# Performance work log

Measured on AMD Instinct MI355X. Metric: run time of the kernel, lower is better.

Reference implementation:

```python
import jax, jax.numpy as jnp
import numpy as np

B, S, D, H = 4, 2048, 1024, 16
HD = D // H
BITS = 8
LEVELS = 2 ** BITS - 1          # number of negative log2 levels
SCALING = 32.0 / 16.0           # lora alpha / rank for 8-bit adapter
NEG_INF = -1e9


def log_fake_quant(x, reduce_axes):
    """Per-channel log-domain fake quantization with straight-through estimator.
    Scale = per-channel max-abs; magnitudes snapped to power-of-two fractions of scale."""
    s = jnp.maximum(jnp.max(jnp.abs(x), axis=reduce_axes, keepdims=True), 1e-8)
    ratio = jnp.clip(jnp.abs(x) / s, 2.0 ** (-LEVELS), 1.0)
    e = jnp.round(jnp.log2(ratio))                      # in [-LEVELS, 0]
    q = jnp.sign(x) * s * jnp.exp2(e)
    return x + jax.lax.stop_gradient(q - x)             # STE


def cpt_linear(x, W, b, lA, lB):
    """CPTLinear: fake-quantized activation/weight GEMM + bias + LoRA on the fp input."""
    xq = log_fake_quant(x, tuple(range(x.ndim - 1)))     # per last-dim channel
    Wq = log_fake_quant(W, (1,))                         # per output row (channel_dim=0)
    out = xq @ Wq.T + b
    return out + (x @ lA @ lB) * SCALING


def setup_inputs() -> dict:
    key = jax.random.key(0)
    ks = jax.random.split(key, 8)
    causal = jnp.tril(jnp.ones((S, S), dtype=bool))
    mask = jnp.where(causal, 0.0, NEG_INF).astype(jnp.float32)[None, None]  # [1,1,S,S]
    return {
        "hidden_states": jax.random.normal(ks[0], (B, S, D), jnp.float32),
        "attention_mask": mask,
        "W_attn": jax.random.normal(ks[1], (3 * D, D), jnp.float32) * 0.02,
        "b_attn": jnp.zeros((3 * D,), jnp.float32),
        "lA_attn": jax.random.normal(ks[2], (D, 16), jnp.float32) * 0.01,
        "lB_attn": jax.random.normal(ks[3], (16, 3 * D), jnp.float32) * 0.01,
        "W_proj": jax.random.normal(ks[4], (D, D), jnp.float32) * 0.02,
        "b_proj": jnp.zeros((D,), jnp.float32),
        "lA_proj": jax.random.normal(ks[5], (D, 16), jnp.float32) * 0.01,
        "lB_proj": jax.random.normal(ks[6], (16, D), jnp.float32) * 0.01,
    }


def reference(hidden_states, attention_mask, W_attn, b_attn, lA_attn, lB_attn,
              W_proj, b_proj, lA_proj, lB_proj):
    qkv = cpt_linear(hidden_states, W_attn, b_attn, lA_attn, lB_attn)  # [B,S,3D]
    q, k, v = jnp.split(qkv, 3, axis=-1)

    def to_heads(t):
        return t.reshape(B, S, H, HD).transpose(0, 2, 1, 3)            # [B,H,S,HD]

    q, k, v = to_heads(q), to_heads(k), to_heads(v)
    scores = jnp.einsum("bhqd,bhkd->bhqk", q, k) / np.float32(np.sqrt(HD))
    scores = scores + attention_mask
    attn = jax.nn.softmax(scores, axis=-1)                             # dropout: eval mode (identity)
    out = jnp.einsum("bhqk,bhkd->bhqd", attn, v)
    out = out.transpose(0, 2, 1, 3).reshape(B, S, D)
    return cpt_linear(out, W_proj, b_proj, lA_proj, lB_proj)
```

## Files before the change

### kernel.cpp

```cpp
#include <hip/hip_runtime.h>

#define SS 2048
#define DD 1024
#define DQKV 3072
#define KP 1088
#define NT64 17
#define MTOT 8192
#define QKSZ ((size_t)MTOT * DD)
#define SCL 0.18033688011112042f

typedef unsigned short us;
typedef __attribute__((ext_vector_type(8))) short bf16x8;
typedef __attribute__((ext_vector_type(4))) float f32x4;
typedef __attribute__((ext_vector_type(4))) unsigned u32x4;

#define WAITVM(N) asm volatile("s_waitcnt vmcnt(" #N ")" ::: "memory")
#define WAITLGKM0 asm volatile("s_waitcnt lgkmcnt(0)" ::: "memory")

__device__ __forceinline__ us f2bf(float f) {
    unsigned u = __float_as_uint(f);
    return (us)((u + 0x7fffu + ((u >> 16) & 1u)) >> 16);
}
__device__ __forceinline__ float bf2f(us h) { return __uint_as_float(((unsigned)h) << 16); }
__device__ __forceinline__ void split2(float q, us& h, us& l) {
    h = f2bf(q); l = f2bf(q - bf2f(h));
}
__device__ __forceinline__ unsigned cvtpk(float lo, float hi) {
    unsigned r;
    asm("v_cvt_pk_bf16_f32 %0, %1, %2" : "=v"(r) : "v"(lo), "v"(hi));
    return r;
}

__device__ __forceinline__ int logq_e(float ax, float s) {
    int e = 0;
    if (ax < s) {
        double r = (double)ax / (double)s;
        int ex;
        double mant = frexp(r, &ex);
        e = (mant >= 0.70710678118654752440) ? ex : ex - 1;
        e = (e < -255) ? -255 : e;
    }
    return e;
}
__device__ __forceinline__ float logq_exact(float x, float s) {
    float ax = fabsf(x);
    if (ax == 0.f) return copysignf(0.f, x);
    return copysignf(ldexpf(s, logq_e(ax, s)), x);
}

__device__ __forceinline__ void gll16(const void* g, void* l) {
    __builtin_amdgcn_global_load_lds(
        (const __attribute__((address_space(1))) void*)g,
        (__attribute__((address_space(3))) void*)l, 16, 0, 0);
}


__global__ void k_zero(unsigned* p, int n) {
    int i = blockIdx.x * 256 + threadIdx.x;
    if (i < n) p[i] = 0u;
}

__global__ void k_colmax(const float* __restrict__ x, unsigned* __restrict__ smax) {
    int c = blockIdx.x * 256 + threadIdx.x;
    int r0 = blockIdx.y * 128;
    float m = 0.f;
    for (int r = 0; r < 128; ++r) m = fmaxf(m, fabsf(x[(size_t)(r0 + r) * DD + c]));
    atomicMax(smax + c, __float_as_uint(m));
}

__global__ __launch_bounds__(256) void k_quant_lora(const float* __restrict__ x,
                                                    const unsigned* __restrict__ smax,
                                                    const float* __restrict__ lA,
                                                    us* __restrict__ xq) {
    __shared__ float red[4][16];
    int m = blockIdx.x, tx = threadIdx.x;
    int lane = tx & 63, w = tx >> 6;
    float4 xv = ((const float4*)(x + (size_t)m * DD))[tx];
    int c = tx * 4;
    float vv[4] = {xv.x, xv.y, xv.z, xv.w};
    ushort4 qh;
    us* ph = (us*)&qh;
#pragma unroll
    for (int j = 0; j < 4; ++j) {
        float s = fmaxf(__uint_as_float(smax[c + j]), 1e-8f);
        float sh = bf2f(f2bf(s));
        float ax = fabsf(vv[j]);
        if (ax == 0.f) ph[j] = (us)((__float_as_uint(vv[j]) >> 16) & 0x8000u);
        else ph[j] = f2bf(copysignf(ldexpf(sh, logq_e(ax, s)), vv[j]));
    }
    *(ushort4*)(xq + (size_t)m * KP + c) = qh;
    float acc[16];
#pragma unroll
    for (int r = 0; r < 16; ++r) acc[r] = 0.f;
#pragma unroll
    for (int j = 0; j < 4; ++j) {
        float xs = vv[j];
        const float4* lr = (const float4*)(lA + (size_t)(c + j) * 16);
        float4 a0 = lr[0], a1 = lr[1], a2 = lr[2], a3 = lr[3];
        acc[0] += xs * a0.x; acc[1] += xs * a0.y; acc[2] += xs * a0.z; acc[3] += xs * a0.w;
        acc[4] += xs * a1.x; acc[5] += xs * a1.y; acc[6] += xs * a1.z; acc[7] += xs * a1.w;
        acc[8] += xs * a2.x; acc[9] += xs * a2.y; acc[10] += xs * a2.z; acc[11] += xs * a2.w;
        acc[12] += xs * a3.x; acc[13] += xs * a3.y; acc[14] += xs * a3.z; acc[15] += xs * a3.w;
    }
#pragma unroll
    for (int msk = 1; msk < 64; msk <<= 1)
#pragma unroll
        for (int r = 0; r < 16; ++r) acc[r] += __shfl_xor(acc[r], msk);
    if (lane == 0)
#pragma unroll
        for (int r = 0; r < 16; ++r) red[w][r] = acc[r];
    __syncthreads();
    if (tx < 16) {
        float v = 2.0f * (red[0][tx] + red[1][tx] + red[2][tx] + red[3][tx]);
        us h, l; split2(v, h, l);
        xq[(size_t)m * KP + 1024 + tx] = h;
        xq[(size_t)m * KP + 1040 + tx] = l;
    } else if (tx == 16) {
        xq[(size_t)m * KP + 1056] = 0x3F80;
    } else if (tx < 48) {
        xq[(size_t)m * KP + 1040 + tx] = 0;
    }
}

__global__ __launch_bounds__(256) void k_quant_w(const float* __restrict__ W, const float* __restrict__ lB,
                                                 const float* __restrict__ bias,
                                                 const unsigned* __restrict__ smax,
                                                 us* __restrict__ wh, us* __restrict__ wl, int Nn) {
    __shared__ float red[4];
    int n = blockIdx.x, tx = threadIdx.x;
    int lane = tx & 63, w = tx >> 6;
    float4 wv = ((const float4*)(W + (size_t)n * DD))[tx];
    float m4 = fmaxf(fmaxf(fabsf(wv.x), fabsf(wv.y)), fmaxf(fabsf(wv.z), fabsf(wv.w)));
#pragma unroll
    for (int msk = 1; msk < 64; msk <<= 1) m4 = fmaxf(m4, __shfl_xor(m4, msk));
    if (lane == 0) red[w] = m4;
    __syncthreads();
    float t = fmaxf(fmaxf(fmaxf(red[0], red[1]), fmaxf(red[2], red[3])), 1e-8f);
    float vv[4] = {wv.x, wv.y, wv.z, wv.w};
    int c = tx * 4;
    ushort4 qh, ql;
    us* ph = (us*)&qh; us* pl = (us*)&ql;
#pragma unroll
    for (int j = 0; j < 4; ++j) {
        float s = fmaxf(__uint_as_float(smax[c + j]), 1e-8f);
        float sh = bf2f(f2bf(s));
        float rho = (s - sh) / sh;
        float q = logq_exact(vv[j], t);
        float wp = q + q * rho;
        split2(wp, ph[j], pl[j]);
    }
    *(ushort4*)(wh + (size_t)n * KP + c) = qh;
    *(ushort4*)(wl + (size_t)n * KP + c) = ql;
    if (tx < 64) {
        us h = 0, l = 0;
        if (tx < 32) { int r = tx & 15; split2(lB[(size_t)r * Nn + n], h, l); }
        else if (tx == 32) split2(bias[n], h, l);
        wh[(size_t)n * KP + 1024 + tx] = h;
        wl[(size_t)n * KP + 1024 + tx] = l;
    }
}


template <int MODE>
__global__ __launch_bounds__(512, 2) void k_gemm(const us* __restrict__ Aq_,
                                                 const us* __restrict__ Bh_, const us* __restrict__ Bl_,
                                                 float* __restrict__ C, int Nn,
                                                 us* __restrict__ Khg, us* __restrict__ Klg,
                                                 float* __restrict__ vbuf) {
    __shared__ us LA[2][16384];
    __shared__ us LBh[2][8192];
    __shared__ us LBl[2][8192];
    int tid = threadIdx.x;
    int bm = blockIdx.x, bn = blockIdx.y;
    int lane = tid & 63, w = tid >> 6;
    int wm = w >> 2, wn = w & 3;
    int l15 = lane & 15, l4 = lane >> 4;
    int srow = tid >> 3;
    int gsrc = ((tid & 7) ^ (srow & 7)) * 8;
    const us* aP  = Aq_ + (size_t)(bm * 256 + srow) * KP + gsrc;
    const us* bhP = Bh_ + (size_t)(bn * 128 + srow) * KP + gsrc;
    const us* blP = Bl_ + (size_t)(bn * 128 + srow) * KP + gsrc;
    f32x4 zero4 = {0.f, 0.f, 0.f, 0.f};
    f32x4 acc[8][2];
#pragma unroll
    for (int i = 0; i < 8; ++i) { acc[i][0] = zero4; acc[i][1] = zero4; }

#define GSTAGE(buf, kt)                                               \
    do {                                                              \
        int k0_ = (kt) * 64;                                          \
        gll16(aP + k0_,                    &LA[(buf)][0]     + tid * 8); \
        gll16(aP + (size_t)64  * KP + k0_, &LA[(buf)][4096]  + tid * 8); \
        gll16(aP + (size_t)128 * KP + k0_, &LA[(buf)][8192]  + tid * 8); \
        gll16(aP + (size_t)192 * KP + k0_, &LA[(buf)][12288] + tid * 8); \
        gll16(bhP + k0_,                   &LBh[(buf)][0]    + tid * 8); \
        gll16(bhP + (size_t)64 * KP + k0_, &LBh[(buf)][4096] + tid * 8); \
        gll16(blP + k0_,                   &LBl[(buf)][0]    + tid * 8); \
        gll16(blP + (size_t)64 * KP + k0_, &LBl[(buf)][4096] + tid * 8); \
    } while (0)

    GSTAGE(0, 0);
    GSTAGE(1, 1);
    WAITVM(8);
    __builtin_amdgcn_s_barrier();
    __builtin_amdgcn_sched_barrier(0);

    int gsw0 = ((l4)     ^ (l15 & 7)) * 8;
    int gsw1 = ((4 + l4) ^ (l15 & 7)) * 8;
    int cur = 0;
    for (int kt = 0; kt < NT64; ++kt) {
        const us* A0  = &LA[cur][0];
        const us* Bh0 = &LBh[cur][0];
        const us* Bl0 = &LBl[cur][0];
        bf16x8 a0[8], b0h[2], b0l[2];
#pragma unroll
        for (int i = 0; i < 8; ++i)
            a0[i] = *(const bf16x8*)(A0 + (wm * 128 + i * 16 + l15) * 64 + gsw0);
#pragma unroll
        for (int i = 0; i < 2; ++i) {
            b0h[i] = *(const bf16x8*)(Bh0 + (wn * 32 + i * 16 + l15) * 64 + gsw0);
            b0l[i] = *(const bf16x8*)(Bl0 + (wn * 32 + i * 16 + l15) * 64 + gsw0);
        }
        __builtin_amdgcn_s_setprio(1);
#pragma unroll
        for (int mi = 0; mi < 8; ++mi)
#pragma unroll
            for (int ni = 0; ni < 2; ++ni) {
                acc[mi][ni] = __builtin_amdgcn_mfma_f32_16x16x32_bf16(a0[mi], b0h[ni], acc[mi][ni], 0, 0, 0);
                acc[mi][ni] = __builtin_amdgcn_mfma_f32_16x16x32_bf16(a0[mi], b0l[ni], acc[mi][ni], 0, 0, 0);
            }
        __builtin_amdgcn_s_setprio(0);
        bf16x8 a1[8], b1h[2], b1l[2];
#pragma unroll
        for (int i = 0; i < 8; ++i)
            a1[i] = *(const bf16x8*)(A0 + (wm * 128 + i * 16 + l15) * 64 + gsw1);
#pragma unroll
        for (int i = 0; i < 2; ++i) {
            b1h[i] = *(const bf16x8*)(Bh0 + (wn * 32 + i * 16 + l15) * 64 + gsw1);
            b1l[i] = *(const bf16x8*)(Bl0 + (wn * 32 + i * 16 + l15) * 64 + gsw1);
        }
        WAITLGKM0;
        __builtin_amdgcn_sched_barrier(0);
        __builtin_amdgcn_s_barrier();
        __builtin_amdgcn_sched_barrier(0);
        if (kt + 2 < NT64) GSTAGE(cur, kt + 2);
        __builtin_amdgcn_s_setprio(1);
#pragma unroll
        for (int mi = 0; mi < 8; ++mi)
#pragma unroll
            for (int ni = 0; ni < 2; ++ni) {
                acc[mi][ni] = __builtin_amdgcn_mfma_f32_16x16x32_bf16(a1[mi], b1h[ni], acc[mi][ni], 0, 0, 0);
                acc[mi][ni] = __builtin_amdgcn_mfma_f32_16x16x32_bf16(a1[mi], b1l[ni], acc[mi][ni], 0, 0, 0);
            }
        __builtin_amdgcn_s_setprio(0);
        if (kt + 2 < NT64) { WAITVM(8); } else { WAITVM(0); }
        __builtin_amdgcn_s_barrier();
        __builtin_amdgcn_sched_barrier(0);
        cur ^= 1;
    }
#undef GSTAGE

    int plane = bn >> 3;
#pragma unroll
    for (int mi = 0; mi < 8; ++mi) {
#pragma unroll
        for (int ni = 0; ni < 2; ++ni) {
            int ncol = bn * 128 + wn * 32 + ni * 16 + l15;
            size_t mbase = (size_t)bm * 256 + wm * 128 + mi * 16 + l4 * 4;
#pragma unroll
            for (int rr = 0; rr < 4; ++rr) {
                float v = acc[mi][ni][rr];
                size_t m = mbase + rr;
                if (MODE == 0) {
                    C[m * (size_t)Nn + ncol] = v;
                } else {
                    int cc = ncol & 1023;
                    if (plane == 0) {
                        C[m * DD + cc] = v;
                    } else if (plane == 2) {
                        vbuf[m * DD + cc] = v;
                    } else {
                        us hh, ll; split2(v * SCL, hh, ll);
                        size_t d = ((size_t)((m >> 11) * 16 + (cc >> 6)) * SS + (m & 2047)) * 64 + (cc & 63);
                        Khg[d] = hh; Klg[d] = ll;
                    }
                }
            }
        }
    }
}


__global__ __launch_bounds__(256) void k_transpose_v(const float* __restrict__ vbuf,
                                                     us* __restrict__ vth, us* __restrict__ vtl) {
    __shared__ us th[64][72], tl[64][72];
    int st = blockIdx.x, bh = blockIdx.y;
    int bb = bh >> 4, h = bh & 15;
    int s0 = st * 64, tid = threadIdx.x;
    int sl = tid >> 2, c0 = (tid & 3) * 16;
    const float* src = vbuf + (size_t)(bb * SS + s0 + sl) * DD + h * 64 + c0;
#pragma unroll
    for (int j4 = 0; j4 < 4; ++j4) {
        float4 v = *(const float4*)(src + j4 * 4);
        float vv[4] = {v.x, v.y, v.z, v.w};
#pragma unroll
        for (int j = 0; j < 4; ++j) {
            us hh, ll; split2(vv[j], hh, ll);
            th[c0 + j4 * 4 + j][sl] = hh;
            tl[c0 + j4 * 4 + j][sl] = ll;
        }
    }
    __syncthreads();
#pragma unroll
    for (int p = 0; p < 2; ++p) {
        int gidx = p * 256 + tid;
        int hd = gidx >> 3, g = gidx & 7;
        int base = (g >> 2) * 32 + (g & 3) * 4;
        ushort4 a, b2, c, d2;
        a.x = th[hd][base];      a.y = th[hd][base + 1];  a.z = th[hd][base + 2];  a.w = th[hd][base + 3];
        b2.x = th[hd][base + 16]; b2.y = th[hd][base + 17]; b2.z = th[hd][base + 18]; b2.w = th[hd][base + 19];
        c.x = tl[hd][base];      c.y = tl[hd][base + 1];  c.z = tl[hd][base + 2];  c.w = tl[hd][base + 3];
        d2.x = tl[hd][base + 16]; d2.y = tl[hd][base + 17]; d2.z = tl[hd][base + 18]; d2.w = tl[hd][base + 19];
        size_t dof = ((size_t)bh * 64 + hd) * SS + s0 + g * 8;
        *(ushort4*)(vth + dof) = a;  *(ushort4*)(vth + dof + 4) = b2;
        *(ushort4*)(vtl + dof) = c;  *(ushort4*)(vtl + dof + 4) = d2;
    }
}


__global__ __launch_bounds__(512, 2) void k_attn(float* qo,
                                                 const us* __restrict__ Khg, const us* __restrict__ Klg,
                                                 const us* __restrict__ vth, const us* __restrict__ vtl) {
    __shared__ us L[2][16384];
    int bh = blockIdx.x;
    int qt = (int)(gridDim.y - 1) - blockIdx.y;
    int b = bh >> 4, h = bh & 15;
    int q0 = qt * 128;
    int tid = threadIdx.x, w = tid >> 6, lane = tid & 63;
    int l15 = lane & 15, l4 = lane >> 4;
    int qw = q0 + w * 16;
    int swz = l15 & 7;

    bf16x8 qh[2], ql[2];
#pragma unroll
    for (int hf = 0; hf < 2; ++hf) {
        const float* qp = qo + (size_t)(b * SS + qw + l15) * DD + h * 64 + hf * 32 + l4 * 8;
        float4 a = *(const float4*)qp;
        float4 c = *(const float4*)(qp + 4);
        float vv[8] = {a.x, a.y, a.z, a.w, c.x, c.y, c.z, c.w};
        bf16x8 hq, lq;
#pragma unroll
        for (int j = 0; j < 8; ++j) {
            us hh = f2bf(vv[j]);
            hq[j] = (short)hh;
            lq[j] = (short)f2bf(vv[j] - bf2f(hh));
        }
        qh[hf] = hq; ql[hf] = lq;
    }

    f32x4 zero4 = {0.f, 0.f, 0.f, 0.f};
    f32x4 of[4];
#pragma unroll
    for (int j = 0; j < 4; ++j) of[j] = zero4;
    float mrow = -1e30f, lrowp = 0.f;

    int r0 = tid >> 3, sl0 = (tid & 7) ^ (r0 & 7);
    int koff0 = (bh * SS + r0) * 64 + sl0 * 8;
    int voff0 = (bh * 64 + r0) * SS + sl0 * 8;

    int ntiles = qt * 2 + 2;

#define STAGE(buf, tt)                                           \
    do {                                                         \
        int kv_ = (tt) * 64;                                     \
        us* D_ = &L[(buf)][0];                                   \
        int kadd_ = kv_ << 6;                                    \
        gll16(Khg + koff0 + kadd_, D_ + tid * 8);                \
        gll16(Klg + koff0 + kadd_, D_ + 4096 + tid * 8);         \
        gll16(vth + voff0 + kv_, D_ + 8192 + tid * 8);           \
        gll16(vtl + voff0 + kv_, D_ + 12288 + tid * 8);          \
    } while (0)

    STAGE(0, 0);
    STAGE(1, 1);
    int cur = 0;

    for (int t = 0; t < ntiles; ++t) {
        int kv0 = t * 64;
        if (t + 1 < ntiles) WAITVM(4); else WAITVM(0);
        __builtin_amdgcn_s_barrier();

        if (kv0 <= qw + 15) {
            const us* Lc = &L[cur][0];

            f32x4 sf[4];
#pragma unroll
            for (int i = 0; i < 4; ++i) sf[i] = zero4;
            __builtin_amdgcn_s_setprio(1);
#pragma unroll
            for (int kb = 0; kb < 4; ++kb) {
                int rbase = (kb * 16 + l15) * 64;
#pragma unroll
                for (int hf = 0; hf < 2; ++hf) {
                    int off = rbase + (((hf * 4 + l4) ^ swz) * 8);
                    bf16x8 kh = *(const bf16x8*)(Lc + off);
                    bf16x8 kl = *(const bf16x8*)(Lc + 4096 + off);
                    sf[kb] = __builtin_amdgcn_mfma_f32_16x16x32_bf16(kh, qh[hf], sf[kb], 0, 0, 0);
                    sf[kb] = __builtin_amdgcn_mfma_f32_16x16x32_bf16(kh, ql[hf], sf[kb], 0, 0, 0);
                    sf[kb] = __builtin_amdgcn_mfma_f32_16x16x32_bf16(kl, qh[hf], sf[kb], 0, 0, 0);
                }
            }
            __builtin_amdgcn_s_setprio(0);

            bool diag = (kv0 + 63 > qw);
            u32x4 PH[2], PL[2];
            {
                float pv[16];
                if (diag) {
                    int qg = qw + l15;
#pragma unroll
                    for (int kb = 0; kb < 4; ++kb)
#pragma unroll
                        for (int rr = 0; rr < 4; ++rr) {
                            int kvg = kv0 + kb * 16 + l4 * 4 + rr;
                            pv[kb * 4 + rr] = (kvg > qg) ? -1e30f : sf[kb][rr];
                        }
                } else {
#pragma unroll
                    for (int kb = 0; kb < 4; ++kb)
#pragma unroll
                        for (int rr = 0; rr < 4; ++rr)
                            pv[kb * 4 + rr] = sf[kb][rr];
                }
                float t0 = fmaxf(fmaxf(pv[0], pv[1]), pv[2]);
                float t1 = fmaxf(fmaxf(pv[3], pv[4]), pv[5]);
                float t2 = fmaxf(fmaxf(pv[6], pv[7]), pv[8]);
                float t3 = fmaxf(fmaxf(pv[9], pv[10]), pv[11]);
                float t4 = fmaxf(fmaxf(pv[12], pv[13]), pv[14]);
                float tmax = fmaxf(fmaxf(fmaxf(t0, t1), fmaxf(t2, t3)), fmaxf(t4, pv[15]));
                tmax = fmaxf(tmax, __shfl_xor(tmax, 16));
                tmax = fmaxf(tmax, __shfl_xor(tmax, 32));
                float mcur = mrow;
                if (!__all(tmax <= mcur + 8.0f)) {
                    float mnew = fmaxf(mcur, tmax);
                    float fac = __builtin_amdgcn_exp2f(mcur - mnew);
                    mrow = mnew; mcur = mnew;
                    lrowp *= fac;
                    float fr0 = __shfl(fac, l4 * 4 + 0);
                    float fr1 = __shfl(fac, l4 * 4 + 1);
                    float fr2 = __shfl(fac, l4 * 4 + 2);
                    float fr3 = __shfl(fac, l4 * 4 + 3);
#pragma unroll
                    for (int hb = 0; hb < 4; ++hb) {
                        of[hb][0] *= fr0; of[hb][1] *= fr1;
                        of[hb][2] *= fr2; of[hb][3] *= fr3;
                    }
                }
                float ps = 0.f;
#pragma unroll
                for (int i = 0; i < 16; ++i) {
                    pv[i] = __builtin_amdgcn_exp2f(pv[i] - mcur);
                    ps += pv[i];
                }
                lrowp += ps;
#pragma unroll
                for (int ks = 0; ks < 2; ++ks)
#pragma unroll
                    for (int c2 = 0; c2 < 4; ++c2) {
                        float p0 = pv[ks * 8 + c2 * 2], p1 = pv[ks * 8 + c2 * 2 + 1];
                        unsigned u = cvtpk(p0, p1);
                        float h0 = __uint_as_float(u << 16);
                        float h1 = __uint_as_float(u & 0xffff0000u);
                        unsigned ul = cvtpk(p0 - h0, p1 - h1);
                        PH[ks][c2] = u; PL[ks][c2] = ul;
                    }
            }

            __builtin_amdgcn_s_setprio(1);
#pragma unroll
            for (int hb = 0; hb < 4; ++hb) {
                int rbase = (hb * 16 + l15) * 64;
#pragma unroll
                for (int ks = 0; ks < 2; ++ks) {
                    int off = rbase + (((ks * 4 + l4) ^ swz) * 8);
                    bf16x8 vh = *(const bf16x8*)(Lc + 8192 + off);
                    bf16x8 vl = *(const bf16x8*)(Lc + 12288 + off);
                    bf16x8 pa = (bf16x8)PH[ks];
                    bf16x8 pb = (bf16x8)PL[ks];
                    of[hb] = __builtin_amdgcn_mfma_f32_16x16x32_bf16(pa, vh, of[hb], 0, 0, 0);
                    of[hb] = __builtin_amdgcn_mfma_f32_16x16x32_bf16(pa, vl, of[hb], 0, 0, 0);
                    of[hb] = __builtin_amdgcn_mfma_f32_16x16x32_bf16(pb, vh, of[hb], 0, 0, 0);
                }
            }
            __builtin_amdgcn_s_setprio(0);
        }

        __builtin_amdgcn_s_barrier();
        if (t + 2 < ntiles) STAGE(cur, t + 2);
        cur ^= 1;
    }
#undef STAGE

    {
        float lr = lrowp;
        lr += __shfl_xor(lr, 16);
        lr += __shfl_xor(lr, 32);
        float linv = 1.f / lr;
        float f0 = __shfl(linv, l4 * 4 + 0);
        float f1 = __shfl(linv, l4 * 4 + 1);
        float f2 = __shfl(linv, l4 * 4 + 2);
        float f3 = __shfl(linv, l4 * 4 + 3);
        int qgb = qw + l4 * 4;
#pragma unroll
        for (int hb = 0; hb < 4; ++hb) {
            int col = h * 64 + hb * 16 + l15;
            qo[((size_t)(b * SS + qgb + 0)) * DD + col] = of[hb][0] * f0;
            qo[((size_t)(b * SS + qgb + 1)) * DD + col] = of[hb][1] * f1;
            qo[((size_t)(b * SS + qgb + 2)) * DD + col] = of[hb][2] * f2;
            qo[((size_t)(b * SS + qgb + 3)) * DD + col] = of[hb][3] * f3;
        }
    }
}


extern "C" void kernel_launch(void* const* d_in, const int* in_sizes, int n_in,
                              void* d_out, int out_size, void* d_ws, size_t ws_size,
                              hipStream_t stream) {
    const float* hidden  = (const float*)d_in[0];
    const float* W_attn  = (const float*)d_in[2];
    const float* b_attn  = (const float*)d_in[3];
    const float* lA_attn = (const float*)d_in[4];
    const float* lB_attn = (const float*)d_in[5];
    const float* W_proj  = (const float*)d_in[6];
    const float* b_proj  = (const float*)d_in[7];
    const float* lA_proj = (const float*)d_in[8];
    const float* lB_proj = (const float*)d_in[9];
    float* out = (float*)d_out;

    char* ws = (char*)d_ws;
    unsigned* s1 = (unsigned*)(ws);
    unsigned* s2 = (unsigned*)(ws + 4096);
    us* xq  = (us*)(ws + 8192);
    us* vth = xq;
    us* wh1 = (us*)(ws + 8192 + 17825792);
    us* wl1 = (us*)(ws + 8192 + 17825792 + 6684672);
    us* wh2 = (us*)(ws + 8192 + 17825792 + 2 * 6684672);
    us* wl2 = (us*)(ws + 8192 + 17825792 + 2 * 6684672 + 2228224);
    char* pbase = ws + 8192 + 17825792 + 2 * 6684672 + 2 * 2228224;
    float* qbuf = (float*)pbase;
    float* vbuf = (float*)(pbase + 33554432);
    us* Khg = (us*)(pbase + 2 * (size_t)33554432);
    us* Klg = (us*)(pbase + 2 * (size_t)33554432 + 16777216);
    us* vtl = (us*)(pbase + 2 * (size_t)33554432 + 2 * (size_t)16777216);

    k_zero<<<8, 256, 0, stream>>>(s1, 2048);

    k_colmax<<<dim3(4, 64), 256, 0, stream>>>(hidden, s1);
    k_quant_lora<<<MTOT, 256, 0, stream>>>(hidden, s1, lA_attn, xq);
    k_quant_w<<<3072, 256, 0, stream>>>(W_attn, lB_attn, b_attn, s1, wh1, wl1, 3072);
    k_gemm<1><<<dim3(32, 24), 512, 0, stream>>>(xq, wh1, wl1, qbuf, DQKV, Khg, Klg, vbuf);

    k_transpose_v<<<dim3(32, 64), 256, 0, stream>>>(vbuf, vth, vtl);
    k_attn<<<dim3(64, 16), 512, 0, stream>>>(qbuf, Khg, Klg, vth, vtl);

    k_colmax<<<dim3(4, 64), 256, 0, stream>>>(qbuf, s2);
    k_quant_lora<<<MTOT, 256, 0, stream>>>(qbuf, s2, lA_proj, xq);
    k_quant_w<<<1024, 256, 0, stream>>>(W_proj, lB_proj, b_proj, s2, wh2, wl2, 1024);
    k_gemm<0><<<dim3(32, 8), 512, 0, stream>>>(xq, wh2, wl2, out, DD, nullptr, nullptr, nullptr);
}
```

Measured before the change: 447.4 us.

## Halve GEMM K-tile to 32 to raise occupancy and use float log-quant

Shrinks the GEMM K-step from 64 to 32, halving LDS buffers so launch bounds can request 4 blocks per CU instead of 2, with a matching XOR swizzle for 32-wide rows. The loop now does one MFMA phase per iteration, with two barriers. The log-quant exponent is computed with a float frexp plus a double-precision squared-boundary correction, replacing the double division. The aim is more resident waves to hide latency, at the cost of twice as many barriers and loop iterations and a tighter register budget that could cause spills with 16 accumulators.

```diff
diff --git a/kernel.cpp b/kernel.cpp
--- a/kernel.cpp
+++ b/kernel.cpp
@@ -4,7 +4,7 @@
 #define DD 1024
 #define DQKV 3072
 #define KP 1088
-#define NT64 17
+#define NT32 34
 #define MTOT 8192
 #define QKSZ ((size_t)MTOT * DD)
 #define SCL 0.18033688011112042f
@@ -34,11 +34,15 @@
 __device__ __forceinline__ int logq_e(float ax, float s) {
     int e = 0;
     if (ax < s) {
-        double r = (double)ax / (double)s;
         int ex;
-        double mant = frexp(r, &ex);
-        e = (mant >= 0.70710678118654752440) ? ex : ex - 1;
-        e = (e < -255) ? -255 : e;
+        float m = frexpf(ax / s, &ex);
+        int k = (m >= 0.70710678f) ? ex : ex - 1;
+        double ax2 = (double)ax * (double)ax;
+        double s2 = (double)s * (double)s;
+        if (ax2 >= ldexp(s2, 2 * k + 1)) k += 1;
+        else if (ax2 < ldexp(s2, 2 * k - 1)) k -= 1;
+        if (k > 0) k = 0;
+        e = (k < -255) ? -255 : k;
     }
     return e;
 }
@@ -162,21 +166,21 @@
 
 
 template <int MODE>
-__global__ __launch_bounds__(512, 2) void k_gemm(const us* __restrict__ Aq_,
+__global__ __launch_bounds__(512, 4) void k_gemm(const us* __restrict__ Aq_,
                                                  const us* __restrict__ Bh_, const us* __restrict__ Bl_,
                                                  float* __restrict__ C, int Nn,
                                                  us* __restrict__ Khg, us* __restrict__ Klg,
                                                  float* __restrict__ vbuf) {
-    __shared__ us LA[2][16384];
-    __shared__ us LBh[2][8192];
-    __shared__ us LBl[2][8192];
+    __shared__ us LA[2][8192];
+    __shared__ us LBh[2][4096];
+    __shared__ us LBl[2][4096];
     int tid = threadIdx.x;
     int bm = blockIdx.x, bn = blockIdx.y;
     int lane = tid & 63, w = tid >> 6;
     int wm = w >> 2, wn = w & 3;
     int l15 = lane & 15, l4 = lane >> 4;
-    int srow = tid >> 3;
-    int gsrc = ((tid & 7) ^ (srow & 7)) * 8;
+    int srow = tid >> 2;
+    int gsrc = ((tid & 3) ^ ((srow ^ (srow >> 2)) & 3)) * 8;
     const us* aP  = Aq_ + (size_t)(bm * 256 + srow) * KP + gsrc;
     const us* bhP = Bh_ + (size_t)(bn * 128 + srow) * KP + gsrc;
     const us* blP = Bl_ + (size_t)(bn * 128 + srow) * KP + gsrc;
@@ -185,41 +189,40 @@
 #pragma unroll
     for (int i = 0; i < 8; ++i) { acc[i][0] = zero4; acc[i][1] = zero4; }
 
-#define GSTAGE(buf, kt)                                               \
-    do {                                                              \
-        int k0_ = (kt) * 64;                                          \
-        gll16(aP + k0_,                    &LA[(buf)][0]     + tid * 8); \
-        gll16(aP + (size_t)64  * KP + k0_, &LA[(buf)][4096]  + tid * 8); \
-        gll16(aP + (size_t)128 * KP + k0_, &LA[(buf)][8192]  + tid * 8); \
-        gll16(aP + (size_t)192 * KP + k0_, &LA[(buf)][12288] + tid * 8); \
-        gll16(bhP + k0_,                   &LBh[(buf)][0]    + tid * 8); \
-        gll16(bhP + (size_t)64 * KP + k0_, &LBh[(buf)][4096] + tid * 8); \
-        gll16(blP + k0_,                   &LBl[(buf)][0]    + tid * 8); \
-        gll16(blP + (size_t)64 * KP + k0_, &LBl[(buf)][4096] + tid * 8); \
+#define GSTAGE(buf, kt)                                                  \
+    do {                                                                 \
+        int k0_ = (kt) * 32;                                             \
+        gll16(aP + k0_,                    &LA[(buf)][0]    + tid * 8);  \
+        gll16(aP + (size_t)128 * KP + k0_, &LA[(buf)][4096] + tid * 8);  \
+        gll16(bhP + k0_,                   &LBh[(buf)][0]   + tid * 8);  \
+        gll16(blP + k0_,                   &LBl[(buf)][0]   + tid * 8);  \
     } while (0)
 
     GSTAGE(0, 0);
     GSTAGE(1, 1);
-    WAITVM(8);
-    __builtin_amdgcn_s_barrier();
-    __builtin_amdgcn_sched_barrier(0);
-
-    int gsw0 = ((l4)     ^ (l15 & 7)) * 8;
-    int gsw1 = ((4 + l4) ^ (l15 & 7)) * 8;
+
+    int gsw = ((l4 ^ ((l15 ^ (l15 >> 2)) & 3))) * 8;
     int cur = 0;
-    for (int kt = 0; kt < NT64; ++kt) {
+    for (int kt = 0; kt < NT32; ++kt) {
+        if (kt + 1 < NT32) { WAITVM(4); } else { WAITVM(0); }
+        __builtin_amdgcn_s_barrier();
         const us* A0  = &LA[cur][0];
         const us* Bh0 = &LBh[cur][0];
         const us* Bl0 = &LBl[cur][0];
         bf16x8 a0[8], b0h[2], b0l[2];
 #pragma unroll
         for (int i = 0; i < 8; ++i)
-            a0[i] = *(const bf16x8*)(A0 + (wm * 128 + i * 16 + l15) * 64 + gsw0);
+            a0[i] = *(const bf16x8*)(A0 + (wm * 128 + i * 16 + l15) * 32 + gsw);
 #pragma unroll
         for (int i = 0; i < 2; ++i) {
-            b0h[i] = *(const bf16x8*)(Bh0 + (wn * 32 + i * 16 + l15) * 64 + gsw0);
-            b0l[i] = *(const bf16x8*)(Bl0 + (wn * 32 + i * 16 + l15) * 64 + gsw0);
+            b0h[i] = *(const bf16x8*)(Bh0 + (wn * 32 + i * 16 + l15) * 32 + gsw);
+            b0l[i] = *(const bf16x8*)(Bl0 + (wn * 32 + i * 16 + l15) * 32 + gsw);
         }
+        WAITLGKM0;
+        __builtin_amdgcn_sched_barrier(0);
+        __builtin_amdgcn_s_barrier();
+        __builtin_amdgcn_sched_barrier(0);
+        if (kt + 2 < NT32) GSTAGE(cur, kt + 2);
         __builtin_amdgcn_s_setprio(1);
 #pragma unroll
         for (int mi = 0; mi < 8; ++mi)
@@ -229,32 +232,6 @@
                 acc[mi][ni] = __builtin_amdgcn_mfma_f32_16x16x32_bf16(a0[mi], b0l[ni], acc[mi][ni], 0, 0, 0);
             }
         __builtin_amdgcn_s_setprio(0);
-        bf16x8 a1[8], b1h[2], b1l[2];
-#pragma unroll
-        for (int i = 0; i < 8; ++i)
-            a1[i] = *(const bf16x8*)(A0 + (wm * 128 + i * 16 + l15) * 64 + gsw1);
-#pragma unroll
-        for (int i = 0; i < 2; ++i) {
-            b1h[i] = *(const bf16x8*)(Bh0 + (wn * 32 + i * 16 + l15) * 64 + gsw1);
-            b1l[i] = *(const bf16x8*)(Bl0 + (wn * 32 + i * 16 + l15) * 64 + gsw1);
-        }
-        WAITLGKM0;
-        __builtin_amdgcn_sched_barrier(0);
-        __builtin_amdgcn_s_barrier();
-        __builtin_amdgcn_sched_barrier(0);
-        if (kt + 2 < NT64) GSTAGE(cur, kt + 2);
-        __builtin_amdgcn_s_setprio(1);
-#pragma unroll
-        for (int mi = 0; mi < 8; ++mi)
-#pragma unroll
-            for (int ni = 0; ni < 2; ++ni) {
-                acc[mi][ni] = __builtin_amdgcn_mfma_f32_16x16x32_bf16(a1[mi], b1h[ni], acc[mi][ni], 0, 0, 0);
-                acc[mi][ni] = __builtin_amdgcn_mfma_f32_16x16x32_bf16(a1[mi], b1l[ni], acc[mi][ni], 0, 0, 0);
-            }
-        __builtin_amdgcn_s_setprio(0);
-        if (kt + 2 < NT64) { WAITVM(8); } else { WAITVM(0); }
-        __builtin_amdgcn_s_barrier();
-        __builtin_amdgcn_sched_barrier(0);
         cur ^= 1;
     }
 #undef GSTAGE
@@ -386,7 +363,7 @@
 
     for (int t = 0; t < ntiles; ++t) {
         int kv0 = t * 64;
-        if (t + 1 < ntiles) WAITVM(4); else WAITVM(0);
+        if (t + 1 < ntiles) { WAITVM(4); } else { WAITVM(0); }
         __builtin_amdgcn_s_barrier();
 
         if (kv0 <= qw + 15) {
```

After: 493.2 us. +10.2%, slower.
